# Performance work log

Hardware: AMD Instinct MI355X
Metric: run time of the kernel (lower is better)

The kernel has to match this reference:

```python
import jax, jax.numpy as jnp
import numpy as np

PI = 3.1415927410125732
N = 4096
VELOCITY = 5e-7
RC = 3.15e-6          # collision radius
RR = 8e-6             # repulsion radius
RO = 2.5e-5           # orientation radius (Ra = inf -> inside_Ra all-true)
ALPHA = PI            # field of view; < 2*pi so within_view masking is active
DT_TRANS = 1.4e-14    # translational diffusion DT
DR = 0.0028
GAMMA = 25.0
DT = 0.2              # timestep dt
COLLISION_ITERS = 3   # fixed-iteration version of recursive solve_collisions
EPS = 1e-14


def _c(x):  # [N,2] real -> complex64
    return jax.lax.complex(x[..., 0], x[..., 1])


def _r(z):  # complex -> [..., 2] real
    return jnp.stack([z.real, z.imag], axis=-1)


def _anglediff(a, b):
    # torch get_anglediff: wrap angle(a)-angle(b) into (-pi, pi)
    diff = jnp.angle(a) - jnp.angle(b)
    diff = jnp.where(diff <= -PI, jnp.mod(diff, PI), diff)
    return diff - (diff >= PI) * (2.0 * PI)


def _cossim(a, b):
    # nn.CosineSimilarity(dim=1, eps=1e-14) on view_as_real of complex vectors
    dot = a.real * b.real + a.imag * b.imag
    na = jnp.sqrt(a.real ** 2 + a.imag ** 2 + 1e-30)
    nb = jnp.sqrt(b.real ** 2 + b.imag ** 2 + 1e-30)
    return dot / (jnp.maximum(na, EPS) * jnp.maximum(nb, EPS))


def setup_inputs() -> dict:
    key = jax.random.key(0)
    k1, k2, k3, k4, k5 = jax.random.split(key, 5)
    positions = jax.random.normal(k1, (N, 2), jnp.float32) * 5e-4
    ang = jax.random.uniform(k2, (N,), jnp.float32, -PI, PI)
    orientations = jnp.stack([jnp.cos(ang), jnp.sin(ang)], axis=-1)  # unit complex
    Deltas = jax.random.uniform(k3, (1,), jnp.float32, 0.1, 0.6)
    rot_noise = jax.random.normal(k4, (N,), jnp.float32)
    trans_noise = jax.random.normal(k5, (N, 2), jnp.float32)
    return {"positions": positions, "orientations": orientations, "Deltas": Deltas,
            "rot_noise": rot_noise, "trans_noise": trans_noise}


def reference(positions, orientations, Deltas, rot_noise, trans_noise):
    p = _c(positions)      # [N] complex positions
    u = _c(orientations)   # [N] complex orientations
    n = p.shape[0]
    eye = jnp.eye(n, dtype=bool)

    # pairwise direction/distance: dirs[i,j] = p_j - p_i
    dirs = p[None, :] - p[:, None]
    dists = jnp.abs(dirs)

    inside_Rr = (dists <= RR) & ~eye
    inside_Ro = dists <= RO + RC
    # inside_Ra with Ra = inf is all-True

    # angle between separation vector and orientation of the *neighbor* j
    ang_diff = _anglediff(dirs, u[None, :])
    in_front = ang_diff < PI / 2
    within_view = ang_diff < ALPHA  # alpha < 2*pi branch active

    cdtype = p.dtype
    mask_rr = (inside_Rr & in_front).astype(cdtype)
    mask_ra = within_view.astype(cdtype)  # inside_Ra all True
    mask_ro = (inside_Ro & within_view).astype(cdtype)

    n_r = mask_rr.real.sum(axis=1)
    S = (mask_rr @ p) / jnp.maximum(n_r, 1.0) - p * jnp.sign(n_r)
    d = -S

    n_a = mask_ra.real.sum(axis=1)
    cms = (mask_ra @ p) / jnp.maximum(n_a, 1.0)
    Ps = cms - p * jnp.sign(n_a)

    orientation_sums = mask_ro @ u

    leftturns = Ps * jnp.exp(1j * Deltas)
    rightturns = Ps * jnp.exp(-1j * Deltas)

    # T >= T_release branch: pick the turn most aligned with neighbor orientations
    left_closer = _cossim(leftturns, orientation_sums) >= _cossim(rightturns, orientation_sums)
    best_turns = jnp.where(left_closer, leftturns, rightturns)

    d_abs = jnp.abs(d)
    d_safe = jnp.where(d_abs > 0, d, jnp.ones((), cdtype))
    best_safe = jnp.where(jnp.abs(best_turns) > 0, best_turns, jnp.ones((), cdtype))
    angle_to_target = jnp.where(d_abs > 0, _anglediff(d_safe, u), _anglediff(best_safe, u))

    # rotational_noise = randn * sqrt(2*DR); rotation = exp(i*(dt*Gamma*DR*sin + noise*sqrt(dt)))
    rot = jnp.exp(1j * (DT * GAMMA * DR * jnp.sin(angle_to_target)
                        + rot_noise * np.float32(np.sqrt(2 * DR)) * np.float32(np.sqrt(DT))))

    # complex-normal translational noise (per-component std 1/sqrt(2)) * sqrt(2*DT) * sqrt(dt)
    tn = _c(trans_noise) * np.float32(np.sqrt(0.5)) * np.float32(np.sqrt(2 * DT_TRANS))
    translation = DT * VELOCITY * u + tn * np.float32(np.sqrt(DT))

    def collide(i, pos):
        dd = pos[None, :] - pos[:, None]
        dd_nd = jnp.where(eye, jnp.ones((), pos.dtype), dd)  # avoid 0/0 on diagonal
        ab = jnp.where(eye, 0.0, jnp.abs(dd_nd))
        coll = ab <= 2 * RC - jnp.eye(n, dtype=ab.dtype)
        safe = jnp.where(coll, ab, 1.0)
        move = jnp.where(coll, dd / safe * ((2.1 * RC - ab) * 0.5), jnp.zeros((), pos.dtype))
        return pos - move.sum(axis=1)

    new_p = jax.lax.fori_loop(0, COLLISION_ITERS, collide, p + translation)
    new_u = u * rot

    # pack the 5 complex outputs as real [5, N, 2]
    return jnp.stack([_r(new_p), _r(new_u), _r(orientation_sums), _r(leftturns), _r(rightturns)], axis=0)
```

## Files before the change

kernel.cpp:

```cpp
#include <hip/hip_runtime.h>
#include <math.h>

#define NPART 4096
#define NBLK  1024
#define NTHR  256
#define IPB   4
#define SMAX  256
#define PPT   (NPART / NTHR)

constexpr float RORC   = (float)(2.5e-5 + 3.15e-6);
constexpr float RORC2  = RORC * RORC;
constexpr float RRF    = 8e-6f;
constexpr float RR2    = RRF * RRF;
constexpr float TWORC  = (float)(2.0 * 3.15e-6);
constexpr float TWORC2 = TWORC * TWORC;
constexpr float C21RC  = (float)(2.1 * 3.15e-6);
constexpr float RCAND2 = 1.6e-9f;
constexpr float C_ROT  = (float)(0.2 * 25.0 * 0.0028);
constexpr float C_RN1  = (float)0.07483314773547883;
constexpr float C_SQDT = (float)0.4472135954999579;
constexpr float C_TRV  = (float)(0.2 * 5e-7);
constexpr float C_HALF = (float)0.7071067811865476;
constexpr float C_SQ2T = (float)1.6733200530681511e-07;
constexpr float EPSF   = 1e-14f;

__global__ __launch_bounds__(NTHR, 6) void fused_all(
        const float2* __restrict__ pos, const float2* __restrict__ ori,
        const float* __restrict__ Deltas, const float* __restrict__ rot_noise,
        const float2* __restrict__ trans_noise, float2* __restrict__ out) {
    __shared__ float    sred[2 * NTHR];
    __shared__ float    res[5][IPB];
    __shared__ unsigned bmap[NPART / 32];
    __shared__ int      Sidx[SMAX];
    __shared__ float4   posS4[SMAX / 2];
    __shared__ int      scnt;
    float2* posS = (float2*)posS4;
    const float4* __restrict__ pos4 = (const float4*)pos;

    const int tid  = threadIdx.x;
    const int il   = tid >> 6;
    const int lane = tid & 63;
    const int gi   = blockIdx.x * IPB + il;

    const float2 pi   = pos[gi];
    const float  delv = Deltas[0];
    float rn_early = 0.f;
    if (tid < IPB) rn_early = rot_noise[blockIdx.x * IPB + tid];
    {
        const float2 ow = ori[tid * PPT];
        const float2 tw = trans_noise[tid * PPT];
        asm volatile("" :: "v"(ow.x), "v"(tw.x));
    }

    if (tid == 0) scnt = IPB;
    if (tid < IPB) Sidx[tid] = blockIdx.x * IPB + tid;
    if (tid < NPART / 32) bmap[tid] = 0u;
    __syncthreads();

    float nr = 0.f, sx = 0.f, sy = 0.f, oxs = 0.f, oys = 0.f;
    auto pair2 = [&](const float4& w, int jbase) {
        const float dx0 = w.x - pi.x, dy0 = w.y - pi.y;
        const float r20 = fmaf(dx0, dx0, dy0 * dy0);
        const float dx1 = w.z - pi.x, dy1 = w.w - pi.y;
        const float r21 = fmaf(dx1, dx1, dy1 * dy1);
        if (r20 <= RCAND2) {
            atomicOr(&bmap[jbase >> 5], 1u << (jbase & 31));
            if (r20 <= RORC2) {
                const float2 uj = ori[jbase];
                oxs += uj.x; oys += uj.y;
                if (r20 <= RR2 && r20 > 0.f) {
                    const float dt_ = fmaf(dx0, uj.x, dy0 * uj.y);
                    const float cr_ = fmaf(dy0, uj.x, -dx0 * uj.y);
                    if (!((dt_ <= 0.f) && (cr_ >= 0.f))) {
                        nr += 1.f; sx += w.x; sy += w.y;
                    }
                }
            }
        }
        if (r21 <= RCAND2) {
            const int j1 = jbase + 1;
            atomicOr(&bmap[j1 >> 5], 1u << (j1 & 31));
            if (r21 <= RORC2) {
                const float2 uj = ori[j1];
                oxs += uj.x; oys += uj.y;
                if (r21 <= RR2 && r21 > 0.f) {
                    const float dt_ = fmaf(dx1, uj.x, dy1 * uj.y);
                    const float cr_ = fmaf(dy1, uj.x, -dx1 * uj.y);
                    if (!((dt_ <= 0.f) && (cr_ >= 0.f))) {
                        nr += 1.f; sx += w.z; sy += w.w;
                    }
                }
            }
        }
    };
    for (int t0 = lane; t0 < NPART / 2; t0 += 256) {
        const float4 w0 = pos4[t0];
        const float4 w1 = pos4[t0 + 64];
        const float4 w2 = pos4[t0 + 128];
        const float4 w3 = pos4[t0 + 192];
        pair2(w0, 2 * t0);
        pair2(w1, 2 * (t0 + 64));
        pair2(w2, 2 * (t0 + 128));
        pair2(w3, 2 * (t0 + 192));
    }
    {
        float vals[5] = {nr, sx, sy, oxs, oys};
        #pragma unroll
        for (int q = 0; q < 5; ++q)
            #pragma unroll
            for (int off = 32; off >= 1; off >>= 1)
                vals[q] += __shfl_down(vals[q], off);
        if (lane == 0) {
            res[0][il] = vals[0]; res[1][il] = vals[1]; res[2][il] = vals[2];
            res[3][il] = vals[3]; res[4][il] = vals[4];
        }
    }

    float mx = 0.f, my = 0.f;
    #pragma unroll
    for (int k = 0; k < PPT; ++k) {
        const float2 v = pos[k * NTHR + tid];
        mx += v.x; my += v.y;
    }
    sred[tid] = mx; sred[NTHR + tid] = my;
    __syncthreads();

    if (tid < 128) {
        sred[tid]        += sred[tid + 128];
        sred[NTHR + tid] += sred[NTHR + tid + 128];
        unsigned bits = bmap[tid];
        if (tid == (int)(blockIdx.x >> 3))
            bits &= ~(0xFu << ((blockIdx.x & 7) * 4));
        while (bits) {
            const int b = __ffs(bits) - 1;
            bits &= bits - 1;
            const int slot = atomicAdd(&scnt, 1);
            if (slot < SMAX) Sidx[slot] = tid * 32 + b;
        }
    }
    __syncthreads();
    const int nS = (scnt < SMAX) ? scnt : SMAX;

    if (tid < 64) {
        sred[tid]        += sred[tid + 64];
        sred[NTHR + tid] += sred[NTHR + tid + 64];
    }
    if (tid < nS) {
        const int p = Sidx[tid];
        const float2 pq = pos[p];
        const float2 uu = ori[p];
        const float2 tn = trans_noise[p];
        posS[tid] = make_float2(
            pq.x + (C_TRV * uu.x + ((tn.x * C_HALF) * C_SQ2T) * C_SQDT),
            pq.y + (C_TRV * uu.y + ((tn.y * C_HALF) * C_SQ2T) * C_SQDT));
    }
    __syncthreads();

    float cmx = 0.f, cmy = 0.f;
    if (il == 0) {
        float vx = sred[lane];
        float vy = sred[NTHR + lane];
        #pragma unroll
        for (int off = 32; off >= 1; off >>= 1) {
            vx += __shfl_down(vx, off);
            vy += __shfl_down(vy, off);
        }
        cmx = __shfl(vx, 0) * (1.f / NPART);
        cmy = __shfl(vy, 0) * (1.f / NPART);
    }

    if (tid < IPB) {
        const int g2 = blockIdx.x * IPB + tid;
        const float2 p = pos[g2];
        const float2 u = ori[g2];
        const float nrv = res[0][tid], sxv = res[1][tid], syv = res[2][tid];
        const float osx = res[3][tid], osy = res[4][tid];

        const float inv = 1.f / fmaxf(nrv, 1.f);
        const float sg  = (nrv > 0.f) ? 1.f : 0.f;
        const float Sx = sxv * inv - p.x * sg;
        const float Sy = syv * inv - p.y * sg;
        const float dxv = -Sx, dyv = -Sy;

        const float Psx = cmx - p.x;
        const float Psy = cmy - p.y;

        float sd, cd;
        sincosf(delv, &sd, &cd);
        const float Lx = Psx * cd - Psy * sd;
        const float Ly = Psx * sd + Psy * cd;
        const float Rx = Psx * cd + Psy * sd;
        const float Ry = Psy * cd - Psx * sd;

        const float no  = fmaxf(sqrtf(osx * osx + osy * osy + 1e-30f), EPSF);
        const float nl  = fmaxf(sqrtf(Lx * Lx + Ly * Ly + 1e-30f), EPSF);
        const float nrr = fmaxf(sqrtf(Rx * Rx + Ry * Ry + 1e-30f), EPSF);
        const float csl = (Lx * osx + Ly * osy) / (nl * no);
        const float csr = (Rx * osx + Ry * osy) / (nrr * no);
        const bool left = (csl >= csr);
        const float bx = left ? Lx : Rx;
        const float by = left ? Ly : Ry;

        float cx, cy;
        if (dxv != 0.f || dyv != 0.f)    { cx = dxv; cy = dyv; }
        else if (bx != 0.f || by != 0.f) { cx = bx;  cy = by;  }
        else                             { cx = 1.f; cy = 0.f; }

        const float dt_ = cx * u.x + cy * u.y;
        const float cr_ = cy * u.x - cx * u.y;
        const float sin_t = cr_ / sqrtf(dt_ * dt_ + cr_ * cr_);

        const float ang = C_ROT * sin_t + (rn_early * C_RN1) * C_SQDT;
        float sa, ca;
        sincosf(ang, &sa, &ca);
        out[1 * NPART + g2] = make_float2(u.x * ca - u.y * sa,
                                          u.x * sa + u.y * ca);
        out[2 * NPART + g2] = make_float2(osx, osy);
        out[3 * NPART + g2] = make_float2(Lx, Ly);
        out[4 * NPART + g2] = make_float2(Rx, Ry);
    }

    for (int pass = 0; pass < 3; ++pass) {
        float px = 0.f, py = 0.f, ax = 0.f, ay = 0.f;
        const bool mv = (tid < nS);
        if (mv) { px = posS[tid].x; py = posS[tid].y; }
        int b = 0;
        for (; b + 4 <= nS; b += 4) {
            const float4 w0 = posS4[(b >> 1)];
            const float4 w1 = posS4[(b >> 1) + 1];
            const float bxs[4] = {w0.x, w0.z, w1.x, w1.z};
            const float bys[4] = {w0.y, w0.w, w1.y, w1.w};
            #pragma unroll
            for (int s = 0; s < 4; ++s) {
                if (mv) {
                    const float dx = bxs[s] - px, dy = bys[s] - py;
                    const float r2 = fmaf(dx, dx, dy * dy);
                    if (r2 <= TWORC2 && r2 > 0.f) {
                        const float ab = sqrtf(r2);
                        const float sc = (C21RC - ab) * 0.5f / ab;
                        ax = fmaf(dx, sc, ax);
                        ay = fmaf(dy, sc, ay);
                    }
                }
            }
        }
        for (; b < nS; ++b) {
            const float2 pb = posS[b];
            if (mv) {
                const float dx = pb.x - px, dy = pb.y - py;
                const float r2 = fmaf(dx, dx, dy * dy);
                if (r2 <= TWORC2 && r2 > 0.f) {
                    const float ab = sqrtf(r2);
                    const float sc = (C21RC - ab) * 0.5f / ab;
                    ax = fmaf(dx, sc, ax);
                    ay = fmaf(dy, sc, ay);
                }
            }
        }
        __syncthreads();
        if (mv) posS[tid] = make_float2(px - ax, py - ay);
        __syncthreads();
    }
    if (tid < IPB)
        out[0 * NPART + blockIdx.x * IPB + tid] = posS[tid];
}

extern "C" void kernel_launch(void* const* d_in, const int* in_sizes, int n_in,
                              void* d_out, int out_size, void* d_ws, size_t ws_size,
                              hipStream_t stream) {
    const float2* pos = (const float2*)d_in[0];
    const float2* ori = (const float2*)d_in[1];
    const float*  del = (const float*)d_in[2];
    const float*  rn  = (const float*)d_in[3];
    const float2* tn  = (const float2*)d_in[4];
    float2* o2 = (float2*)d_out;
    (void)d_ws; (void)ws_size;

    fused_all<<<dim3(NBLK), dim3(NTHR), 0, stream>>>(pos, ori, del, rn, tn, o2);
}
```

Baseline: 84.55 us.

## Build candidate list inline during scan and hoist mean reduction before it

Candidate indices now go into the shared list directly during the pairwise scan, using the atomicOr return value, which removes the separate bitmap-walk phase and one barrier. The block's own bits are seeded into the bitmap up front. The center-of-mass partial sums move before the scan, the scan loop is simplified to stride-64 with unroll 2 and an early skip when both pairs are far, and the collision loop drops its per-thread mask by parking inactive threads at a far sentinel position. Launch bounds drop from 6 to 4 waves, which allows more registers at the cost of occupancy, and candidate ordering in the list becomes nondeterministic.

```diff
diff --git a/kernel.cpp b/kernel.cpp
--- a/kernel.cpp
+++ b/kernel.cpp
@@ -24,7 +24,7 @@
 constexpr float C_SQ2T = (float)1.6733200530681511e-07;
 constexpr float EPSF   = 1e-14f;
 
-__global__ __launch_bounds__(NTHR, 6) void fused_all(
+__global__ __launch_bounds__(NTHR, 4) void fused_all(
         const float2* __restrict__ pos, const float2* __restrict__ ori,
         const float* __restrict__ Deltas, const float* __restrict__ rot_noise,
         const float2* __restrict__ trans_noise, float2* __restrict__ out) {
@@ -40,33 +40,54 @@
     const int tid  = threadIdx.x;
     const int il   = tid >> 6;
     const int lane = tid & 63;
-    const int gi   = blockIdx.x * IPB + il;
+    const int base = blockIdx.x * IPB;
+    const int gi   = base + il;
 
     const float2 pi   = pos[gi];
     const float  delv = Deltas[0];
     float rn_early = 0.f;
-    if (tid < IPB) rn_early = rot_noise[blockIdx.x * IPB + tid];
+    if (tid < IPB) rn_early = rot_noise[base + tid];
     {
-        const float2 ow = ori[tid * PPT];
-        const float2 tw = trans_noise[tid * PPT];
-        asm volatile("" :: "v"(ow.x), "v"(tw.x));
+        const float2 ow = ori[tid * 16];
+        const float2 tw = trans_noise[tid * 16];
+        asm volatile("" :: "v"(ow.x), "v"(ow.y), "v"(tw.x), "v"(tw.y));
     }
 
     if (tid == 0) scnt = IPB;
-    if (tid < IPB) Sidx[tid] = blockIdx.x * IPB + tid;
-    if (tid < NPART / 32) bmap[tid] = 0u;
+    if (tid < IPB) Sidx[tid] = base + tid;
+    if (tid < NPART / 32) {
+        const int seedw = base >> 5;
+        bmap[tid] = (tid == seedw) ? (0xFu << (base & 31)) : 0u;
+    }
+
+    float mx = 0.f, my = 0.f;
+    #pragma unroll
+    for (int k = 0; k < PPT; ++k) {
+        const float2 v = pos[k * NTHR + tid];
+        mx += v.x; my += v.y;
+    }
+    sred[tid] = mx; sred[NTHR + tid] = my;
     __syncthreads();
 
     float nr = 0.f, sx = 0.f, sy = 0.f, oxs = 0.f, oys = 0.f;
-    auto pair2 = [&](const float4& w, int jbase) {
+    #pragma unroll 2
+    for (int t = lane; t < NPART / 2; t += 64) {
+        const float4 w = pos4[t];
         const float dx0 = w.x - pi.x, dy0 = w.y - pi.y;
         const float r20 = fmaf(dx0, dx0, dy0 * dy0);
         const float dx1 = w.z - pi.x, dy1 = w.w - pi.y;
         const float r21 = fmaf(dx1, dx1, dy1 * dy1);
+        if (fminf(r20, r21) > RCAND2) continue;
         if (r20 <= RCAND2) {
-            atomicOr(&bmap[jbase >> 5], 1u << (jbase & 31));
+            const int j = 2 * t;
+            const unsigned bit = 1u << (j & 31);
+            const unsigned old = atomicOr(&bmap[j >> 5], bit);
+            if (!(old & bit)) {
+                const int slot = atomicAdd(&scnt, 1);
+                if (slot < SMAX) Sidx[slot] = j;
+            }
             if (r20 <= RORC2) {
-                const float2 uj = ori[jbase];
+                const float2 uj = ori[j];
                 oxs += uj.x; oys += uj.y;
                 if (r20 <= RR2 && r20 > 0.f) {
                     const float dt_ = fmaf(dx0, uj.x, dy0 * uj.y);
@@ -78,10 +99,15 @@
             }
         }
         if (r21 <= RCAND2) {
-            const int j1 = jbase + 1;
-            atomicOr(&bmap[j1 >> 5], 1u << (j1 & 31));
+            const int j = 2 * t + 1;
+            const unsigned bit = 1u << (j & 31);
+            const unsigned old = atomicOr(&bmap[j >> 5], bit);
+            if (!(old & bit)) {
+                const int slot = atomicAdd(&scnt, 1);
+                if (slot < SMAX) Sidx[slot] = j;
+            }
             if (r21 <= RORC2) {
-                const float2 uj = ori[j1];
+                const float2 uj = ori[j];
                 oxs += uj.x; oys += uj.y;
                 if (r21 <= RR2 && r21 > 0.f) {
                     const float dt_ = fmaf(dx1, uj.x, dy1 * uj.y);
@@ -92,16 +118,6 @@
                 }
             }
         }
-    };
-    for (int t0 = lane; t0 < NPART / 2; t0 += 256) {
-        const float4 w0 = pos4[t0];
-        const float4 w1 = pos4[t0 + 64];
-        const float4 w2 = pos4[t0 + 128];
-        const float4 w3 = pos4[t0 + 192];
-        pair2(w0, 2 * t0);
-        pair2(w1, 2 * (t0 + 64));
-        pair2(w2, 2 * (t0 + 128));
-        pair2(w3, 2 * (t0 + 192));
     }
     {
         float vals[5] = {nr, sx, sy, oxs, oys};
@@ -115,35 +131,12 @@
             res[3][il] = vals[3]; res[4][il] = vals[4];
         }
     }
-
-    float mx = 0.f, my = 0.f;
-    #pragma unroll
-    for (int k = 0; k < PPT; ++k) {
-        const float2 v = pos[k * NTHR + tid];
-        mx += v.x; my += v.y;
-    }
-    sred[tid] = mx; sred[NTHR + tid] = my;
-    __syncthreads();
-
+    __syncthreads();
+
+    const int nS = (scnt < SMAX) ? scnt : SMAX;
     if (tid < 128) {
         sred[tid]        += sred[tid + 128];
         sred[NTHR + tid] += sred[NTHR + tid + 128];
-        unsigned bits = bmap[tid];
-        if (tid == (int)(blockIdx.x >> 3))
-            bits &= ~(0xFu << ((blockIdx.x & 7) * 4));
-        while (bits) {
-            const int b = __ffs(bits) - 1;
-            bits &= bits - 1;
-            const int slot = atomicAdd(&scnt, 1);
-            if (slot < SMAX) Sidx[slot] = tid * 32 + b;
-        }
-    }
-    __syncthreads();
-    const int nS = (scnt < SMAX) ? scnt : SMAX;
-
-    if (tid < 64) {
-        sred[tid]        += sred[tid + 64];
-        sred[NTHR + tid] += sred[NTHR + tid + 64];
     }
     if (tid < nS) {
         const int p = Sidx[tid];
@@ -156,6 +149,12 @@
     }
     __syncthreads();
 
+    if (tid < 64) {
+        sred[tid]        += sred[tid + 64];
+        sred[NTHR + tid] += sred[NTHR + tid + 64];
+    }
+    __syncthreads();
+
     float cmx = 0.f, cmy = 0.f;
     if (il == 0) {
         float vx = sred[lane];
@@ -170,7 +169,7 @@
     }
 
     if (tid < IPB) {
-        const int g2 = blockIdx.x * IPB + tid;
+        const int g2 = base + tid;
         const float2 p = pos[g2];
         const float2 u = ori[g2];
         const float nrv = res[0][tid], sxv = res[1][tid], syv = res[2][tid];
@@ -221,7 +220,7 @@
     }
 
     for (int pass = 0; pass < 3; ++pass) {
-        float px = 0.f, py = 0.f, ax = 0.f, ay = 0.f;
+        float px = 1e9f, py = 1e9f, ax = 0.f, ay = 0.f;
         const bool mv = (tid < nS);
         if (mv) { px = posS[tid].x; py = posS[tid].y; }
         int b = 0;
@@ -232,22 +231,7 @@
             const float bys[4] = {w0.y, w0.w, w1.y, w1.w};
             #pragma unroll
             for (int s = 0; s < 4; ++s) {
-                if (mv) {
-                    const float dx = bxs[s] - px, dy = bys[s] - py;
-                    const float r2 = fmaf(dx, dx, dy * dy);
-                    if (r2 <= TWORC2 && r2 > 0.f) {
-                        const float ab = sqrtf(r2);
-                        const float sc = (C21RC - ab) * 0.5f / ab;
-                        ax = fmaf(dx, sc, ax);
-                        ay = fmaf(dy, sc, ay);
-                    }
-                }
-            }
-        }
-        for (; b < nS; ++b) {
-            const float2 pb = posS[b];
-            if (mv) {
-                const float dx = pb.x - px, dy = pb.y - py;
+                const float dx = bxs[s] - px, dy = bys[s] - py;
                 const float r2 = fmaf(dx, dx, dy * dy);
                 if (r2 <= TWORC2 && r2 > 0.f) {
                     const float ab = sqrtf(r2);
@@ -257,12 +241,23 @@
                 }
             }
         }
+        for (; b < nS; ++b) {
+            const float2 pb = posS[b];
+            const float dx = pb.x - px, dy = pb.y - py;
+            const float r2 = fmaf(dx, dx, dy * dy);
+            if (r2 <= TWORC2 && r2 > 0.f) {
+                const float ab = sqrtf(r2);
+                const float sc = (C21RC - ab) * 0.5f / ab;
+                ax = fmaf(dx, sc, ax);
+                ay = fmaf(dy, sc, ay);
+            }
+        }
         __syncthreads();
         if (mv) posS[tid] = make_float2(px - ax, py - ay);
         __syncthreads();
     }
     if (tid < IPB)
-        out[0 * NPART + blockIdx.x * IPB + tid] = posS[tid];
+        out[0 * NPART + base + tid] = posS[tid];
 }
 
 extern "C" void kernel_launch(void* const* d_in, const int* in_sizes, int n_in,
```

Measured after the change: 85.00 us. No clear change (+0.5%).
